# Kernel optimization log

Hardware: AMD Instinct MI355X
Metric: run time of the kernel (lower is better)

The kernel has to match this reference:

```python
import jax, jax.numpy as jnp
import numpy as np

B, S, D_MODEL, N_HEADS = 4, 2048, 1024, 16
HEAD = D_MODEL // N_HEADS  # 64


def setup_inputs() -> dict:
    key = jax.random.key(0)
    ks = jax.random.split(key, 9)
    s = 1.0 / np.sqrt(D_MODEL)
    return {
        "query": jax.random.normal(ks[0], (B, S, D_MODEL), jnp.float32),
        "key_in": jax.random.normal(ks[1], (B, S, D_MODEL), jnp.float32),
        "value": jax.random.normal(ks[2], (B, S, D_MODEL), jnp.float32),
        "Wq": jax.random.normal(ks[3], (D_MODEL, D_MODEL), jnp.float32) * s,
        "bq": jnp.zeros((D_MODEL,), jnp.float32),
        "Wk": jax.random.normal(ks[4], (D_MODEL, D_MODEL), jnp.float32) * s,
        "bk": jnp.zeros((D_MODEL,), jnp.float32),
        "Wv": jax.random.normal(ks[5], (D_MODEL, D_MODEL), jnp.float32) * s,
        "bv": jnp.zeros((D_MODEL,), jnp.float32),
    }


def reference(query, key_in, value, Wq, bq, Wk, bk, Wv, bv):
    # Dense projections (Keras Dense: x @ W + b)
    q = query @ Wq + bq     # [B,S,D]
    k = key_in @ Wk + bk    # [B,S,D]
    v = value @ Wv + bv     # [B,S,D]
    # split heads -> [B,S,H,Dh]
    q = q.reshape(B, S, N_HEADS, HEAD)
    k = k.reshape(B, S, N_HEADS, HEAD)
    v = v.reshape(B, S, N_HEADS, HEAD)
    scale = 1.0 / jnp.sqrt(jnp.float32(HEAD))
    # full attention matrix [B,H,Sq,Sk] (faithful to original un-fused form)
    scores = jnp.einsum('bqhd,bkhd->bhqk', q, k) * scale
    alpha = jax.nn.softmax(scores, axis=-1)
    ctx = jnp.einsum('bhqk,bkhd->bqhd', alpha, v)  # [B,Sq,H,Dh]
    return ctx.reshape(B, S, D_MODEL)
```

## Files before the change

kernel.cpp:

```cpp
#include <hip/hip_runtime.h>
#include <hip/hip_bf16.h>

#define S_LEN 2048
#define DM    1024
#define NH    16
#define HD    64

typedef __attribute__((ext_vector_type(8))) short short8;
typedef __attribute__((ext_vector_type(4))) short short4v;
typedef __attribute__((ext_vector_type(4))) float f32x4;

__device__ __forceinline__ short f2bf(float f) {
    union { float f; unsigned u; } x; x.f = f;
    unsigned u = x.u;
    return (short)((u + 0x7FFFu + ((u >> 16) & 1u)) >> 16);
}
__device__ __forceinline__ short f2bf_ru(float f) {
    return (short)((__float_as_uint(f) + 0x8000u) >> 16);
}
__device__ __forceinline__ unsigned pk2bf(float a, float b) {
    unsigned ua = __float_as_uint(a) + 0x8000u;
    unsigned ub = __float_as_uint(b) + 0x8000u;
    return (ua >> 16) | (ub & 0xFFFF0000u);
}
__device__ __forceinline__ float fexp2(float x) {
#if __has_builtin(__builtin_amdgcn_exp2f)
    return __builtin_amdgcn_exp2f(x);
#else
    return exp2f(x);
#endif
}
__device__ __forceinline__ void gload_lds16(const void* g, void* l) {
    __builtin_amdgcn_global_load_lds(
        (const __attribute__((address_space(1))) unsigned int*)g,
        (__attribute__((address_space(3))) unsigned int*)l, 16, 0, 0);
}

__global__ void wt_kernel(const float* __restrict__ Wq, const float* __restrict__ Wk,
                          const float* __restrict__ Wv, short* __restrict__ wt_base) {
    __shared__ float t[32][33];
    const float* W = (blockIdx.z == 0) ? Wq : (blockIdx.z == 1 ? Wk : Wv);
    short* WT = wt_base + (size_t)blockIdx.z * DM * DM;
    int kb = blockIdx.x * 32, nb = blockIdx.y * 32;
    int tx = threadIdx.x, ty = threadIdx.y;
#pragma unroll
    for (int r = 0; r < 4; r++)
        t[ty + 8 * r][tx] = W[(size_t)(kb + ty + 8 * r) * DM + nb + tx];
    __syncthreads();
#pragma unroll
    for (int r = 0; r < 4; r++)
        WT[(size_t)(nb + ty + 8 * r) * DM + kb + tx] = f2bf(t[tx][ty + 8 * r]);
}

__global__ __launch_bounds__(256, 3) void projf_kernel(
        const float* __restrict__ Xq, const float* __restrict__ Xk,
        const float* __restrict__ Xv, const short* __restrict__ WT3,
        const float* __restrict__ bq, const float* __restrict__ bk,
        const float* __restrict__ bv,
        short* __restrict__ Qh, short* __restrict__ Kh, short* __restrict__ Vt,
        float qscale) {
    __shared__ __align__(16) short As[2][128 * 32];
    __shared__ __align__(16) short Bs[2][128 * 32];
    const int bid = blockIdx.x;
    const int swz = (bid & 7) * 192 + (bid >> 3);
    const int nx = swz & 7;
    const int my = (swz >> 3) & 63;
    const int z  = swz >> 9;

    const float* X = (z == 0) ? Xq : (z == 1) ? Xk : Xv;
    const short* WT = WT3 + (size_t)z * DM * DM;
    const float* bias = (z == 0) ? bq : (z == 1) ? bk : bv;
    short* out = (z == 0) ? Qh : (z == 1) ? Kh : Vt;
    const float scale = (z == 0) ? qscale : 1.0f;
    const int mode = (z == 2);

    const int tid = threadIdx.x;
    const int lane = tid & 63, w = tid >> 6;
    const int l15 = lane & 15, quad = lane >> 4;
    const int n0 = nx * 128, m0 = my * 128;
    const int wm = (w & 1) * 64, wn = (w >> 1) * 64;
    const int arow = tid >> 3;
    const int ako  = (tid & 7) * 4;

    const float* xb = X + (size_t)m0 * DM;

    f32x4 acc[4][4];
#pragma unroll
    for (int i = 0; i < 4; i++)
#pragma unroll
        for (int j = 0; j < 4; j++) { acc[i][j][0] = 0.f; acc[i][j][1] = 0.f; acc[i][j][2] = 0.f; acc[i][j][3] = 0.f; }

    float4 araw[4];
#pragma unroll
    for (int it = 0; it < 4; it++)
        araw[it] = *(const float4*)(xb + (size_t)(it * 32 + arow) * DM + ako);
#pragma unroll
    for (int it = 0; it < 2; it++) {
        int c = it * 256 + tid;
        int row = c >> 2, ko = (c & 3) * 8;
        gload_lds16(WT + (size_t)(n0 + row) * DM + ko, Bs[0] + c * 8);
    }
#pragma unroll
    for (int it = 0; it < 4; it++) {
        int row = it * 32 + arow;
        uint2 p; p.x = pk2bf(araw[it].x, araw[it].y); p.y = pk2bf(araw[it].z, araw[it].w);
        *(uint2*)(As[0] + row * 32 + ako) = p;
    }

    for (int t = 0; t < 32; t++) {
        const int bi = t & 1;
        const int kn = t * 32 + 32;
        __syncthreads();

        short8 af[4], bf[4];
#pragma unroll
        for (int i = 0; i < 4; i++)
            af[i] = *(const short8*)(As[bi] + (wm + i * 16 + l15) * 32 + quad * 8);
#pragma unroll
        for (int j = 0; j < 4; j++)
            bf[j] = *(const short8*)(Bs[bi] + (wn + j * 16 + l15) * 32 + quad * 8);

        if (t < 31) {
#pragma unroll
            for (int it = 0; it < 4; it++)
                araw[it] = *(const float4*)(xb + (size_t)(it * 32 + arow) * DM + kn + ako);
#pragma unroll
            for (int it = 0; it < 2; it++) {
                int c = it * 256 + tid;
                int row = c >> 2, ko = (c & 3) * 8;
                gload_lds16(WT + (size_t)(n0 + row) * DM + kn + ko, Bs[bi ^ 1] + c * 8);
            }
        }

#pragma unroll
        for (int i = 0; i < 4; i++)
#pragma unroll
            for (int j = 0; j < 4; j++)
                acc[i][j] = __builtin_amdgcn_mfma_f32_16x16x32_bf16(af[i], bf[j], acc[i][j], 0, 0, 0);

        if (t < 31) {
#pragma unroll
            for (int it = 0; it < 4; it++) {
                int row = it * 32 + arow;
                uint2 p; p.x = pk2bf(araw[it].x, araw[it].y); p.y = pk2bf(araw[it].z, araw[it].w);
                *(uint2*)(As[bi ^ 1] + row * 32 + ako) = p;
            }
        }
    }

#pragma unroll
    for (int j = 0; j < 4; j++) {
        int col = n0 + wn + j * 16 + l15;
        float bv_ = bias[col];
        int h = col >> 6, d = col & 63;
#pragma unroll
        for (int i = 0; i < 4; i++) {
            int rowbase = m0 + wm + i * 16 + quad * 4;
            int bb = rowbase >> 11, s0 = rowbase & 2047;
            if (mode == 0) {
#pragma unroll
                for (int r = 0; r < 4; r++)
                    out[((size_t)(bb * NH + h) * S_LEN + (s0 + r)) * HD + d] =
                        f2bf((acc[i][j][r] + bv_) * scale);
            } else {
                short4v pk;
#pragma unroll
                for (int r = 0; r < 4; r++) pk[r] = f2bf((acc[i][j][r] + bv_) * scale);
                *(short4v*)(out + ((size_t)(bb * NH + h) * HD + d) * S_LEN + s0) = pk;
            }
        }
    }
}

__global__ __launch_bounds__(256, 3) void attn_kernel(
        const short* __restrict__ Q, const short* __restrict__ K,
        const short* __restrict__ V, float* __restrict__ out) {
    __shared__ __align__(16) short Ks[2][2][64][32];
    __shared__ __align__(16) short Vs[2][2][64][32];
    __shared__ __align__(16) short ps[4][2][16 * 72];
    const int bid = blockIdx.x;
    const int swz = (bid & 7) * 128 + (bid >> 3);
    const int qi = swz & 15;
    const int h  = (swz >> 4) & 15;
    const int b  = swz >> 8;

    const int tid = threadIdx.x;
    const int lane = tid & 63, w = tid >> 6;
    const int l15 = lane & 15, quad = lane >> 4;
    const int q0 = qi * 128;
    const size_t bh = (size_t)(b * NH + h);
    const short* qp = Q + bh * S_LEN * HD;
    const short* kp = K + bh * S_LEN * HD;
    const short* vp = V + bh * (size_t)HD * S_LEN;

    short8 qa[2][2];
#pragma unroll
    for (int s = 0; s < 2; s++) {
        const short* qr = qp + (size_t)(q0 + w * 32 + s * 16 + l15) * HD + quad * 8;
        qa[s][0] = *(const short8*)(qr);
        qa[s][1] = *(const short8*)(qr + 32);
    }

    f32x4 o[2][4];
    float lsum[2][4];
#pragma unroll
    for (int s = 0; s < 2; s++)
#pragma unroll
        for (int d = 0; d < 4; d++) {
            o[s][d][0] = 0.f; o[s][d][1] = 0.f; o[s][d][2] = 0.f; o[s][d][3] = 0.f;
            lsum[s][d] = 0.f;
        }

    auto stageKV = [&](int kt, int bi) {
        short* kd = &Ks[bi][0][0][0];
        short* vd = &Vs[bi][0][0][0];
#pragma unroll
        for (int it = 0; it < 2; it++) {
            int c = it * 256 + tid;
            int half = c >> 8, row = (c >> 2) & 63, chunk = c & 3;
            int co = half * 32 + chunk * 8;
            gload_lds16(kp + (size_t)(kt + row) * HD + co, kd + c * 8);
            gload_lds16(vp + (size_t)row * S_LEN + kt + co, vd + c * 8);
        }
    };

    stageKV(0, 0);

    for (int t = 0; t < 32; t++) {
        const int bi = t & 1;
        __syncthreads();
        if (t < 31) stageKV((t + 1) << 6, bi ^ 1);

        short8 kf[4][2];
#pragma unroll
        for (int nb = 0; nb < 4; nb++) {
            kf[nb][0] = *(const short8*)(&Ks[bi][0][nb * 16 + l15][quad * 8]);
            kf[nb][1] = *(const short8*)(&Ks[bi][1][nb * 16 + l15][quad * 8]);
        }
        f32x4 sacc[2][4];
#pragma unroll
        for (int nb = 0; nb < 4; nb++)
#pragma unroll
            for (int s = 0; s < 2; s++) {
                f32x4 zz; zz[0] = 0.f; zz[1] = 0.f; zz[2] = 0.f; zz[3] = 0.f;
                zz = __builtin_amdgcn_mfma_f32_16x16x32_bf16(qa[s][0], kf[nb][0], zz, 0, 0, 0);
                sacc[s][nb] = __builtin_amdgcn_mfma_f32_16x16x32_bf16(qa[s][1], kf[nb][1], zz, 0, 0, 0);
            }
#pragma unroll
        for (int s = 0; s < 2; s++)
#pragma unroll
            for (int r = 0; r < 4; r++)
#pragma unroll
                for (int nb = 0; nb < 4; nb++) {
                    float p = fexp2(sacc[s][nb][r]);
                    lsum[s][r] += p;
                    ps[w][s][(quad * 4 + r) * 72 + nb * 16 + l15] = f2bf_ru(p);
                }
        asm volatile("s_waitcnt lgkmcnt(0)" ::: "memory");
        short8 pa[2][2];
#pragma unroll
        for (int s = 0; s < 2; s++) {
            pa[s][0] = *(const short8*)(&ps[w][s][l15 * 72 + quad * 8]);
            pa[s][1] = *(const short8*)(&ps[w][s][l15 * 72 + 32 + quad * 8]);
        }
#pragma unroll
        for (int dd = 0; dd < 4; dd++) {
            short8 v0 = *(const short8*)(&Vs[bi][0][dd * 16 + l15][quad * 8]);
            short8 v1 = *(const short8*)(&Vs[bi][1][dd * 16 + l15][quad * 8]);
#pragma unroll
            for (int s = 0; s < 2; s++) {
                o[s][dd] = __builtin_amdgcn_mfma_f32_16x16x32_bf16(pa[s][0], v0, o[s][dd], 0, 0, 0);
                o[s][dd] = __builtin_amdgcn_mfma_f32_16x16x32_bf16(pa[s][1], v1, o[s][dd], 0, 0, 0);
            }
        }
    }

#pragma unroll
    for (int s = 0; s < 2; s++) {
#pragma unroll
        for (int r = 0; r < 4; r++) {
            float l = lsum[s][r];
            l += __shfl_xor(l, 1);
            l += __shfl_xor(l, 2);
            l += __shfl_xor(l, 4);
            l += __shfl_xor(l, 8);
            lsum[s][r] = 1.f / l;
        }
        float* orow = out + ((size_t)b * S_LEN + q0 + w * 32 + s * 16 + quad * 4) * DM + h * HD + l15;
#pragma unroll
        for (int r = 0; r < 4; r++)
#pragma unroll
            for (int dd = 0; dd < 4; dd++)
                orow[(size_t)r * DM + dd * 16] = o[s][dd][r] * lsum[s][r];
    }
}

extern "C" void kernel_launch(void* const* d_in, const int* in_sizes, int n_in,
                              void* d_out, int out_size, void* d_ws, size_t ws_size,
                              hipStream_t stream) {
    const float* query  = (const float*)d_in[0];
    const float* key_in = (const float*)d_in[1];
    const float* value  = (const float*)d_in[2];
    const float* Wq = (const float*)d_in[3];
    const float* bq = (const float*)d_in[4];
    const float* Wk = (const float*)d_in[5];
    const float* bk = (const float*)d_in[6];
    const float* Wv = (const float*)d_in[7];
    const float* bv = (const float*)d_in[8];

    short* wt = (short*)d_ws;
    short* Qh = wt + 3 * 1048576;
    short* Kh = Qh + 8388608;
    short* Vt = Kh + 8388608;
    float* out = (float*)d_out;

    const float QSCALE = 0.125f * 1.44269504088896340736f;

    wt_kernel<<<dim3(32, 32, 3), dim3(32, 8), 0, stream>>>(Wq, Wk, Wv, wt);
    projf_kernel<<<dim3(1536), 256, 0, stream>>>(query, key_in, value, wt,
                                                 bq, bk, bv, Qh, Kh, Vt, QSCALE);
    attn_kernel<<<dim3(1024), 256, 0, stream>>>(Qh, Kh, Vt, out);
}
```

Baseline: 368.5 us.

## Stage fp32 A tiles to LDS asynchronously and swizzle LDS layouts

In the projection GEMM, the activation tile is now copied as fp32 straight into shared memory with direct global-to-LDS loads, instead of going through registers with a bf16 pack before the LDS write. The bf16 conversion moves to fragment-read time. Both the A and B tiles get XOR-swizzled chunk layouts to reduce LDS bank conflicts. This frees registers and removes the register round trip for A, at the cost of twice the LDS for A and duplicated conversion work across waves that share rows.

```diff
diff --git a/kernel.cpp b/kernel.cpp
--- a/kernel.cpp
+++ b/kernel.cpp
@@ -59,7 +59,7 @@
         const float* __restrict__ bv,
         short* __restrict__ Qh, short* __restrict__ Kh, short* __restrict__ Vt,
         float qscale) {
-    __shared__ __align__(16) short As[2][128 * 32];
+    __shared__ __align__(16) float Asf[2][128 * 32];
     __shared__ __align__(16) short Bs[2][128 * 32];
     const int bid = blockIdx.x;
     const int swz = (bid & 7) * 192 + (bid >> 3);
@@ -79,8 +79,6 @@
     const int l15 = lane & 15, quad = lane >> 4;
     const int n0 = nx * 128, m0 = my * 128;
     const int wm = (w & 1) * 64, wn = (w >> 1) * 64;
-    const int arow = tid >> 3;
-    const int ako  = (tid & 7) * 4;
 
     const float* xb = X + (size_t)m0 * DM;
 
@@ -90,46 +88,54 @@
 #pragma unroll
         for (int j = 0; j < 4; j++) { acc[i][j][0] = 0.f; acc[i][j][1] = 0.f; acc[i][j][2] = 0.f; acc[i][j][3] = 0.f; }
 
-    float4 araw[4];
-#pragma unroll
-    for (int it = 0; it < 4; it++)
-        araw[it] = *(const float4*)(xb + (size_t)(it * 32 + arow) * DM + ako);
-#pragma unroll
-    for (int it = 0; it < 2; it++) {
-        int c = it * 256 + tid;
-        int row = c >> 2, ko = (c & 3) * 8;
-        gload_lds16(WT + (size_t)(n0 + row) * DM + ko, Bs[0] + c * 8);
-    }
-#pragma unroll
-    for (int it = 0; it < 4; it++) {
-        int row = it * 32 + arow;
-        uint2 p; p.x = pk2bf(araw[it].x, araw[it].y); p.y = pk2bf(araw[it].z, araw[it].w);
-        *(uint2*)(As[0] + row * 32 + ako) = p;
-    }
+    auto stageA = [&](int k0, int bi) {
+#pragma unroll
+        for (int it = 0; it < 4; it++) {
+            int c = it * 256 + tid;
+            int row = c >> 3, ch = c & 7;
+            int gch = ch ^ (row & 7);
+            gload_lds16(xb + (size_t)row * DM + k0 + gch * 4, Asf[bi] + c * 4);
+        }
+    };
+    auto stageB = [&](int k0, int bi) {
+#pragma unroll
+        for (int it = 0; it < 2; it++) {
+            int c = it * 256 + tid;
+            int row = c >> 2, ch = c & 3;
+            int gch = ch ^ (row & 3);
+            gload_lds16(WT + (size_t)(n0 + row) * DM + k0 + gch * 8, Bs[bi] + c * 8);
+        }
+    };
+
+    stageA(0, 0);
+    stageB(0, 0);
 
     for (int t = 0; t < 32; t++) {
         const int bi = t & 1;
-        const int kn = t * 32 + 32;
         __syncthreads();
+        if (t < 31) {
+            stageA(t * 32 + 32, bi ^ 1);
+            stageB(t * 32 + 32, bi ^ 1);
+        }
 
         short8 af[4], bf[4];
 #pragma unroll
-        for (int i = 0; i < 4; i++)
-            af[i] = *(const short8*)(As[bi] + (wm + i * 16 + l15) * 32 + quad * 8);
-#pragma unroll
-        for (int j = 0; j < 4; j++)
-            bf[j] = *(const short8*)(Bs[bi] + (wn + j * 16 + l15) * 32 + quad * 8);
-
-        if (t < 31) {
-#pragma unroll
-            for (int it = 0; it < 4; it++)
-                araw[it] = *(const float4*)(xb + (size_t)(it * 32 + arow) * DM + kn + ako);
-#pragma unroll
-            for (int it = 0; it < 2; it++) {
-                int c = it * 256 + tid;
-                int row = c >> 2, ko = (c & 3) * 8;
-                gload_lds16(WT + (size_t)(n0 + row) * DM + kn + ko, Bs[bi ^ 1] + c * 8);
-            }
+        for (int i = 0; i < 4; i++) {
+            int row = wm + i * 16 + l15;
+            int c0 = (quad * 2) ^ (row & 7);
+            int c1 = (quad * 2 + 1) ^ (row & 7);
+            f32x4 lo = *(const f32x4*)(Asf[bi] + row * 32 + c0 * 4);
+            f32x4 hi = *(const f32x4*)(Asf[bi] + row * 32 + c1 * 4);
+            uint4 u;
+            u.x = pk2bf(lo[0], lo[1]); u.y = pk2bf(lo[2], lo[3]);
+            u.z = pk2bf(hi[0], hi[1]); u.w = pk2bf(hi[2], hi[3]);
+            af[i] = *(short8*)&u;
+        }
+#pragma unroll
+        for (int j = 0; j < 4; j++) {
+            int row = wn + j * 16 + l15;
+            int cc = quad ^ (row & 3);
+            bf[j] = *(const short8*)(Bs[bi] + row * 32 + cc * 8);
         }
 
 #pragma unroll
@@ -137,15 +143,6 @@
 #pragma unroll
             for (int j = 0; j < 4; j++)
                 acc[i][j] = __builtin_amdgcn_mfma_f32_16x16x32_bf16(af[i], bf[j], acc[i][j], 0, 0, 0);
-
-        if (t < 31) {
-#pragma unroll
-            for (int it = 0; it < 4; it++) {
-                int row = it * 32 + arow;
-                uint2 p; p.x = pk2bf(araw[it].x, araw[it].y); p.y = pk2bf(araw[it].z, araw[it].w);
-                *(uint2*)(As[bi ^ 1] + row * 32 + ako) = p;
-            }
-        }
     }
 
 #pragma unroll
```

Result: no change. 370.2 us (+0.5%).
